# Kernel optimization log

Hardware: AMD Instinct MI355X
Metric: run time of the kernel (lower is better)

## Reference

```python
import jax, jax.numpy as jnp
import numpy as np

DIM = 1024
E = 8
N = 4096
HID = 4 * DIM
THRESHOLD = 0.3


def setup_inputs() -> dict:
    key = jax.random.key(0)
    ks = jax.random.split(key, 8)
    s = 0.02
    return {
        "x": jax.random.normal(ks[0], (N, DIM), dtype=jnp.float32),
        "expert_inputs": jax.random.normal(ks[1], (E, N, DIM), dtype=jnp.float32),
        "wg": jax.random.normal(ks[2], (DIM, E), dtype=jnp.float32) * s,
        "bg": jnp.zeros((E,), dtype=jnp.float32),
        "w1": jax.random.normal(ks[3], (E, DIM, HID), dtype=jnp.float32) * s,
        "b1": jnp.zeros((E, HID), dtype=jnp.float32),
        "w2": jax.random.normal(ks[4], (E, HID, DIM), dtype=jnp.float32) * s,
        "b2": jnp.zeros((E, DIM), dtype=jnp.float32),
    }


def reference(x, expert_inputs, wg, bg, w1, b1, w2, b2):
    # Gate: softmax over experts. [N, E]
    gate_scores = jax.nn.softmax(x @ wg + bg, axis=-1)

    # Experts: FeedForward(dim, dim, mult=4) = Linear -> GELU -> Linear, batched over E.
    h = jax.nn.gelu(jnp.einsum('end,edh->enh', expert_inputs, w1) + b1[:, None, :],
                    approximate=False)  # [E, N, HID]
    expert_outputs = jnp.einsum('enh,ehd->end', h, w2) + b2[:, None, :]  # [E, N, D]
    expert_outputs = jnp.transpose(expert_outputs, (1, 0, 2))  # [N, E, D]

    # Threshold mask + renormalized weighted combine.
    mask = gate_scores >= THRESHOLD
    masked_scores = gate_scores * mask.astype(gate_scores.dtype)
    normed = masked_scores / (masked_scores.sum(axis=1, keepdims=True) + 1e-6)
    fused = jnp.einsum('ne,ned->nd', normed, expert_outputs)  # [N, D]

    # Fallback: rows with no expert above threshold take the top-1 expert output.
    top1 = jnp.argmax(gate_scores, axis=1)  # [N]
    fallback = jnp.take_along_axis(expert_outputs, top1[:, None, None], axis=1)[:, 0, :]
    fb_mask = (mask.sum(axis=1) == 0)[:, None]
    fused = jnp.where(fb_mask, fallback, fused)
    return fused, gate_scores
```

## Files before the change

kernel.cpp:

```cpp
#include <hip/hip_runtime.h>
#include <hip/hip_bf16.h>
#include <cstdint>

#define N_TOK 4096
#define DIM_  1024
#define HID_  4096
#define NEXP  8
#define HHALF 2048
#define CAP   (3 * N_TOK)

typedef __attribute__((ext_vector_type(8))) short short8;
typedef __attribute__((ext_vector_type(4))) float f32x4;

__device__ __forceinline__ unsigned short f32_to_bf16(float f) {
    union { float f; uint32_t u; } v;
    v.f = f;
    uint32_t r = (v.u + 0x7fffu + ((v.u >> 16) & 1u)) >> 16;
    return (unsigned short)r;
}

__device__ __forceinline__ float gelu_exact(float x) {
    return 0.5f * x * (1.0f + erff(x * 0.70710678118654752440f));
}

__device__ __forceinline__ void gl_lds16(const unsigned short* g, unsigned short* l) {
    __builtin_amdgcn_global_load_lds(
        (const __attribute__((address_space(1))) void*)g,
        (__attribute__((address_space(3))) void*)l, 16, 0, 0);
}

__global__ __launch_bounds__(256)
void zero_init_kernel(float* __restrict__ fused, int* __restrict__ cnt)
{
    const int b = blockIdx.x;
    if (b < N_TOK) {
        float4* p = (float4*)(fused + (size_t)b * DIM_);
        p[threadIdx.x] = make_float4(0.f, 0.f, 0.f, 0.f);
    } else if (threadIdx.x < NEXP) {
        cnt[threadIdx.x] = 0;
    }
}

__global__ __launch_bounds__(256)
void gate_kernel(const float* __restrict__ x, const float* __restrict__ wg,
                 const float* __restrict__ bg, float* __restrict__ gates,
                 float* __restrict__ wts, int* __restrict__ cnt)
{
    const int wave = threadIdx.x >> 6;
    const int lane = threadIdx.x & 63;
    const int n = blockIdx.x * 4 + wave;
    float acc[NEXP];
#pragma unroll
    for (int e = 0; e < NEXP; e++) acc[e] = 0.0f;
    const float4* xr = (const float4*)(x + (size_t)n * DIM_);
#pragma unroll
    for (int j = 0; j < 4; j++) {
        const int k4 = lane + j * 64;
        const float4 v = xr[k4];
        const float* wr = wg + (size_t)k4 * 4 * NEXP;
#pragma unroll
        for (int e = 0; e < NEXP; e++)
            acc[e] += v.x * wr[e] + v.y * wr[NEXP + e] +
                      v.z * wr[2 * NEXP + e] + v.w * wr[3 * NEXP + e];
    }
#pragma unroll
    for (int e = 0; e < NEXP; e++) {
#pragma unroll
        for (int off = 32; off > 0; off >>= 1)
            acc[e] += __shfl_xor(acc[e], off, 64);
    }
    if (lane == 0) {
        float z[NEXP];
#pragma unroll
        for (int e = 0; e < NEXP; e++) z[e] = acc[e] + bg[e];
        float m = z[0];
#pragma unroll
        for (int e = 1; e < NEXP; e++) m = fmaxf(m, z[e]);
        float p[NEXP], s = 0.0f;
#pragma unroll
        for (int e = 0; e < NEXP; e++) { p[e] = __expf(z[e] - m); s += p[e]; }
        const float invs = 1.0f / s;
        float g[NEXP];
        int top = 0;
#pragma unroll
        for (int e = 0; e < NEXP; e++) {
            g[e] = p[e] * invs;
            gates[(size_t)n * NEXP + e] = g[e];
            if (g[e] > g[top]) top = e;
        }
        float w[NEXP], sm = 0.0f;
        int c = 0;
#pragma unroll
        for (int e = 0; e < NEXP; e++) {
            const bool mk = (g[e] >= 0.3f);
            const float ms = mk ? g[e] : 0.0f;
            sm += ms; c += mk ? 1 : 0;
            w[e] = ms;
        }
        if (c == 0) {
#pragma unroll
            for (int e = 0; e < NEXP; e++) w[e] = 0.0f;
            w[top] = 1.0f;
        } else {
            const float inv = 1.0f / (sm + 1e-6f);
#pragma unroll
            for (int e = 0; e < NEXP; e++) w[e] *= inv;
        }
#pragma unroll
        for (int e = 0; e < NEXP; e++) {
            wts[(size_t)n * NEXP + e] = w[e];
            if (w[e] > 0.0f) atomicAdd(&cnt[e], 1);
        }
    }
}

__global__ void offsets_kernel(const int* __restrict__ cnt, int* __restrict__ off,
                               int* __restrict__ cnt2)
{
    if (threadIdx.x == 0) {
        int a = 0;
        for (int e = 0; e < NEXP; e++) { off[e] = a; a += cnt[e]; cnt2[e] = 0; }
    }
}

__global__ __launch_bounds__(256)
void build_list_kernel(const float* __restrict__ wts, const int* __restrict__ off,
                       int* __restrict__ cnt2, int* __restrict__ gidx,
                       float* __restrict__ wpk)
{
    const int n = blockIdx.x * 256 + threadIdx.x;
    if (n >= N_TOK) return;
#pragma unroll
    for (int e = 0; e < NEXP; e++) {
        const float w = wts[(size_t)n * NEXP + e];
        if (w > 0.0f) {
            const int slot = atomicAdd(&cnt2[e], 1);
            const int g = off[e] + slot;
            gidx[g] = n;
            wpk[g] = w;
        }
    }
}

__global__ __launch_bounds__(256)
void gather_cvt_kernel(const float* __restrict__ ei, const int* __restrict__ cnt,
                       const int* __restrict__ off, const int* __restrict__ gidx,
                       unsigned short* __restrict__ xg)
{
    const int e = blockIdx.y;
    const int ne = cnt[e];
    const int i0 = blockIdx.x * 8;
    if (i0 >= ne) return;
    const int grp = threadIdx.x >> 5;
    const int l32 = threadIdx.x & 31;
    const int i = i0 + grp;
    if (i >= ne) return;
    const int o = off[e];
    const float* src = ei + ((size_t)e * N_TOK + gidx[o + i]) * DIM_;
    unsigned short* dst = xg + (size_t)(o + i) * DIM_;
#pragma unroll
    for (int j = 0; j < 8; j++) {
        const int c = (l32 + j * 32) * 4;
        const float4 v = *(const float4*)(src + c);
        ushort4 u;
        u.x = f32_to_bf16(v.x); u.y = f32_to_bf16(v.y);
        u.z = f32_to_bf16(v.z); u.w = f32_to_bf16(v.w);
        *(ushort4*)(dst + c) = u;
    }
}

__global__ __launch_bounds__(256)
void transpose_cvt3(const float* __restrict__ w1, const float* __restrict__ w2,
                    unsigned short* __restrict__ w1t, unsigned short* __restrict__ w2t)
{
    __shared__ __align__(16) unsigned short t[64 * 64];
    const int z = blockIdx.y;
    const float* src;
    unsigned short* dst;
    int C, R, cb, rb;
    if (z < NEXP) {
        src = w1 + (size_t)z * DIM_ * HID_;
        dst = w1t + (size_t)z * DIM_ * HID_;
        C = HID_; R = DIM_;
        cb = blockIdx.x & 63; rb = blockIdx.x >> 6;
    } else {
        src = w2 + (size_t)(z - NEXP) * HID_ * DIM_;
        dst = w2t + (size_t)(z - NEXP) * HID_ * DIM_;
        C = DIM_; R = HID_;
        cb = blockIdx.x & 15; rb = blockIdx.x >> 4;
    }
    const int c0 = cb * 64, r0 = rb * 64;
    const int tid = threadIdx.x;

    const int rB = (tid >> 4) * 4;
    const int cB = (tid & 15) * 4;
    float vv[4][4];
#pragma unroll
    for (int p = 0; p < 4; p++) {
        const float4 v = *(const float4*)(src + (size_t)(r0 + rB + p) * C + c0 + cB);
        vv[p][0] = v.x; vv[p][1] = v.y; vv[p][2] = v.z; vv[p][3] = v.w;
    }
#pragma unroll
    for (int k = 0; k < 4; k++) {
        const int c = cB + k;
        const int s = (c >> 3) & 7;
        const int addr = c * 64 + (((rB >> 3) ^ s) << 3) + (rB & 7);
        ushort4 q;
        q.x = f32_to_bf16(vv[0][k]);
        q.y = f32_to_bf16(vv[1][k]);
        q.z = f32_to_bf16(vv[2][k]);
        q.w = f32_to_bf16(vv[3][k]);
        *(ushort4*)(t + addr) = q;
    }
    __syncthreads();
#pragma unroll
    for (int it = 0; it < 2; it++) {
        const int c = (tid >> 3) + it * 32;
        const int g = tid & 7;
        const int s = (c >> 3) & 7;
        const short8 v8 = *(const short8*)(t + c * 64 + ((g ^ s) << 3));
        *(short8*)(dst + (size_t)(c0 + c) * R + r0 + g * 8) = v8;
    }
}

__global__ __launch_bounds__(256)
void gemm1_k(const unsigned short* __restrict__ xg, const unsigned short* __restrict__ w1t,
             const float* __restrict__ b1, unsigned short* __restrict__ hg,
             const int* __restrict__ cnt, const int* __restrict__ off, int h0)
{
    const int e = blockIdx.z;
    const int ne = cnt[e];
    const int rowBase = blockIdx.y * 128;
    if (rowBase >= ne) return;
    const int o = off[e];
    const int colBase = blockIdx.x * 128;

    __shared__ __align__(16) unsigned short sA[128 * 32];
    __shared__ __align__(16) unsigned short sB[128 * 32];
    const int tid  = threadIdx.x;
    const int lane = tid & 63;
    const int wave = tid >> 6;
    const int wr = wave >> 1, wc = wave & 1;

    f32x4 acc[4][4];
#pragma unroll
    for (int i = 0; i < 4; i++)
#pragma unroll
        for (int j = 0; j < 4; j++)
#pragma unroll
            for (int r = 0; r < 4; r++) acc[i][j][r] = 0.0f;

    const int sr = tid >> 2;
    const int sc = (tid & 3) << 3;
    const int rowA0 = min(rowBase + sr, ne - 1);
    const int rowA1 = min(rowBase + 64 + sr, ne - 1);
    const unsigned short* ga0 = xg + (size_t)(o + rowA0) * DIM_ + sc;
    const unsigned short* ga1 = xg + (size_t)(o + rowA1) * DIM_ + sc;
    const unsigned short* gb0 = w1t + ((size_t)e * HID_ + h0 + colBase + sr) * DIM_ + sc;
    const unsigned short* gb1 = gb0 + (size_t)64 * DIM_;
    unsigned short* la0 = sA + tid * 8;
    unsigned short* la1 = sA + 2048 + tid * 8;
    unsigned short* lb0 = sB + tid * 8;
    unsigned short* lb1 = sB + 2048 + tid * 8;

    const int aoff = (wr * 64 + (lane & 15)) * 32 + ((lane >> 4) << 3);
    const int boff = (wc * 64 + (lane & 15)) * 32 + ((lane >> 4) << 3);

    for (int k0 = 0; k0 < DIM_; k0 += 32) {
        gl_lds16(ga0 + k0, la0);
        gl_lds16(ga1 + k0, la1);
        gl_lds16(gb0 + k0, lb0);
        gl_lds16(gb1 + k0, lb1);
        __syncthreads();
        short8 av[4], bv[4];
#pragma unroll
        for (int i = 0; i < 4; i++) av[i] = *(const short8*)(sA + aoff + i * 16 * 32);
#pragma unroll
        for (int j = 0; j < 4; j++) bv[j] = *(const short8*)(sB + boff + j * 16 * 32);
#pragma unroll
        for (int i = 0; i < 4; i++)
#pragma unroll
            for (int j = 0; j < 4; j++)
                acc[i][j] = __builtin_amdgcn_mfma_f32_16x16x32_bf16(av[i], bv[j], acc[i][j], 0, 0, 0);
        __syncthreads();
    }

    const int crow = rowBase + wr * 64 + ((lane >> 4) << 2);
    const int ccol = colBase + wc * 64 + (lane & 15);
#pragma unroll
    for (int i = 0; i < 4; i++) {
#pragma unroll
        for (int j = 0; j < 4; j++) {
            const int col = ccol + j * 16;
            const float b = b1[(size_t)e * HID_ + h0 + col];
#pragma unroll
            for (int r = 0; r < 4; r++) {
                const int row = crow + i * 16 + r;
                if (row < ne) {
                    const float v = acc[i][j][r] + b;
                    hg[(size_t)(o + row) * HHALF + col] = f32_to_bf16(gelu_exact(v));
                }
            }
        }
    }
}

__global__ __launch_bounds__(256)
void gemm2_k(const unsigned short* __restrict__ hg, const unsigned short* __restrict__ w2t,
             const float* __restrict__ b2, float* __restrict__ fused,
             const int* __restrict__ cnt, const int* __restrict__ off,
             const int* __restrict__ gidx, const float* __restrict__ wpk, int h0)
{
    const int e = blockIdx.z;
    const int ne = cnt[e];
    const int rowBase = blockIdx.y * 128;
    if (rowBase >= ne) return;
    const int o = off[e];
    const int colBase = (blockIdx.x & 7) * 128;
    const int kc = blockIdx.x >> 3;
    const int kbeg = kc * (HHALF / 2);

    __shared__ __align__(16) unsigned short sA[128 * 32];
    __shared__ __align__(16) unsigned short sB[128 * 32];
    const int tid  = threadIdx.x;
    const int lane = tid & 63;
    const int wave = tid >> 6;
    const int wr = wave >> 1, wc = wave & 1;

    f32x4 acc[4][4];
#pragma unroll
    for (int i = 0; i < 4; i++)
#pragma unroll
        for (int j = 0; j < 4; j++)
#pragma unroll
            for (int r = 0; r < 4; r++) acc[i][j][r] = 0.0f;

    const int sr = tid >> 2;
    const int sc = (tid & 3) << 3;
    const int rowA0 = min(rowBase + sr, ne - 1);
    const int rowA1 = min(rowBase + 64 + sr, ne - 1);
    const unsigned short* ga0 = hg + (size_t)(o + rowA0) * HHALF + kbeg + sc;
    const unsigned short* ga1 = hg + (size_t)(o + rowA1) * HHALF + kbeg + sc;
    const unsigned short* gb0 = w2t + ((size_t)e * DIM_ + colBase + sr) * HID_ + h0 + kbeg + sc;
    const unsigned short* gb1 = gb0 + (size_t)64 * HID_;
    unsigned short* la0 = sA + tid * 8;
    unsigned short* la1 = sA + 2048 + tid * 8;
    unsigned short* lb0 = sB + tid * 8;
    unsigned short* lb1 = sB + 2048 + tid * 8;

    const int aoff = (wr * 64 + (lane & 15)) * 32 + ((lane >> 4) << 3);
    const int boff = (wc * 64 + (lane & 15)) * 32 + ((lane >> 4) << 3);

    for (int k0 = 0; k0 < HHALF / 2; k0 += 32) {
        gl_lds16(ga0 + k0, la0);
        gl_lds16(ga1 + k0, la1);
        gl_lds16(gb0 + k0, lb0);
        gl_lds16(gb1 + k0, lb1);
        __syncthreads();
        short8 av[4], bv[4];
#pragma unroll
        for (int i = 0; i < 4; i++) av[i] = *(const short8*)(sA + aoff + i * 16 * 32);
#pragma unroll
        for (int j = 0; j < 4; j++) bv[j] = *(const short8*)(sB + boff + j * 16 * 32);
#pragma unroll
        for (int i = 0; i < 4; i++)
#pragma unroll
            for (int j = 0; j < 4; j++)
                acc[i][j] = __builtin_amdgcn_mfma_f32_16x16x32_bf16(av[i], bv[j], acc[i][j], 0, 0, 0);
        __syncthreads();
    }

    const int crow = rowBase + wr * 64 + ((lane >> 4) << 2);
    const int ccol = colBase + wc * 64 + (lane & 15);
    const int addBias = (h0 == 0 && kc == 0);
#pragma unroll
    for (int i = 0; i < 4; i++) {
#pragma unroll
        for (int j = 0; j < 4; j++) {
            const int col = ccol + j * 16;
            const float b = addBias ? b2[(size_t)e * DIM_ + col] : 0.0f;
#pragma unroll
            for (int r = 0; r < 4; r++) {
                const int row = crow + i * 16 + r;
                if (row < ne) {
                    const float w = wpk[o + row];
                    const int orow = gidx[o + row];
                    atomicAdd(&fused[(size_t)orow * DIM_ + col], w * (acc[i][j][r] + b));
                }
            }
        }
    }
}

extern "C" void kernel_launch(void* const* d_in, const int* in_sizes, int n_in,
                              void* d_out, int out_size, void* d_ws, size_t ws_size,
                              hipStream_t stream)
{
    const float* x  = (const float*)d_in[0];
    const float* ei = (const float*)d_in[1];
    const float* wg = (const float*)d_in[2];
    const float* bg = (const float*)d_in[3];
    const float* w1 = (const float*)d_in[4];
    const float* b1 = (const float*)d_in[5];
    const float* w2 = (const float*)d_in[6];
    const float* b2 = (const float*)d_in[7];

    float* fused = (float*)d_out;
    float* gates = fused + (size_t)N_TOK * DIM_;

    unsigned short* xg  = (unsigned short*)d_ws;
    unsigned short* hg  = xg  + (size_t)CAP * DIM_;
    unsigned short* w1t = hg  + (size_t)CAP * HHALF;
    unsigned short* w2t = w1t + (size_t)NEXP * HID_ * DIM_;
    float* wts = (float*)(w2t + (size_t)NEXP * DIM_ * HID_);
    float* wpk = wts + (size_t)N_TOK * NEXP;
    int* gidx  = (int*)(wpk + CAP);
    int* cnt   = gidx + CAP;
    int* off   = cnt + NEXP;
    int* cnt2  = off + NEXP;

    zero_init_kernel<<<N_TOK + 1, 256, 0, stream>>>(fused, cnt);
    gate_kernel<<<N_TOK / 4, 256, 0, stream>>>(x, wg, bg, gates, wts, cnt);
    offsets_kernel<<<1, 64, 0, stream>>>(cnt, off, cnt2);
    build_list_kernel<<<N_TOK / 256, 256, 0, stream>>>(wts, off, cnt2, gidx, wpk);

    gather_cvt_kernel<<<dim3(N_TOK / 8, NEXP), 256, 0, stream>>>(ei, cnt, off, gidx, xg);
    transpose_cvt3<<<dim3(1024, 16), 256, 0, stream>>>(w1, w2, w1t, w2t);

    for (int h0 = 0; h0 < HID_; h0 += HHALF) {
        gemm1_k<<<dim3(HHALF / 128, N_TOK / 128, NEXP), 256, 0, stream>>>(
            xg, w1t, b1, hg, cnt, off, h0);
        gemm2_k<<<dim3(16, N_TOK / 128, NEXP), 256, 0, stream>>>(
            hg, w2t, b2, fused, cnt, off, gidx, wpk, h0);
    }
}
```

Before: 677.6 us.

## Double-buffer LDS in expert GEMMs and batch four tiles per transpose block

Both expert GEMM kernels now use two LDS buffers, so the async global-to-LDS loads for the next K slice are issued before the MFMAs on the current slice, with an explicit vmcnt wait and barrier. The aim is to overlap global memory latency with matrix compute instead of stalling on every K step. Separately, the weight transpose/convert kernel has each block handle four 64x64 tiles, with all loads issued up front and a quarter as many blocks launched, to raise memory-level parallelism per block. The cost is doubled LDS use per GEMM block, which may lower occupancy, and hand-written waitcnt logic that relies on how the compiler orders the loads.

```diff
diff --git a/kernel.cpp b/kernel.cpp
--- a/kernel.cpp
+++ b/kernel.cpp
@@ -177,49 +177,58 @@
     const int z = blockIdx.y;
     const float* src;
     unsigned short* dst;
-    int C, R, cb, rb;
+    int C, R, cmask, cshift;
     if (z < NEXP) {
         src = w1 + (size_t)z * DIM_ * HID_;
         dst = w1t + (size_t)z * DIM_ * HID_;
-        C = HID_; R = DIM_;
-        cb = blockIdx.x & 63; rb = blockIdx.x >> 6;
+        C = HID_; R = DIM_; cmask = 63; cshift = 6;
     } else {
         src = w2 + (size_t)(z - NEXP) * HID_ * DIM_;
         dst = w2t + (size_t)(z - NEXP) * HID_ * DIM_;
-        C = DIM_; R = HID_;
-        cb = blockIdx.x & 15; rb = blockIdx.x >> 4;
-    }
-    const int c0 = cb * 64, r0 = rb * 64;
+        C = DIM_; R = HID_; cmask = 15; cshift = 4;
+    }
     const int tid = threadIdx.x;
-
     const int rB = (tid >> 4) * 4;
     const int cB = (tid & 15) * 4;
-    float vv[4][4];
-#pragma unroll
-    for (int p = 0; p < 4; p++) {
-        const float4 v = *(const float4*)(src + (size_t)(r0 + rB + p) * C + c0 + cB);
-        vv[p][0] = v.x; vv[p][1] = v.y; vv[p][2] = v.z; vv[p][3] = v.w;
-    }
-#pragma unroll
-    for (int k = 0; k < 4; k++) {
-        const int c = cB + k;
-        const int s = (c >> 3) & 7;
-        const int addr = c * 64 + (((rB >> 3) ^ s) << 3) + (rB & 7);
-        ushort4 q;
-        q.x = f32_to_bf16(vv[0][k]);
-        q.y = f32_to_bf16(vv[1][k]);
-        q.z = f32_to_bf16(vv[2][k]);
-        q.w = f32_to_bf16(vv[3][k]);
-        *(ushort4*)(t + addr) = q;
-    }
-    __syncthreads();
-#pragma unroll
-    for (int it = 0; it < 2; it++) {
-        const int c = (tid >> 3) + it * 32;
-        const int g = tid & 7;
-        const int s = (c >> 3) & 7;
-        const short8 v8 = *(const short8*)(t + c * 64 + ((g ^ s) << 3));
-        *(short8*)(dst + (size_t)(c0 + c) * R + r0 + g * 8) = v8;
+
+    int c0[4], r0[4];
+#pragma unroll
+    for (int tt = 0; tt < 4; tt++) {
+        const int id = blockIdx.x * 4 + tt;
+        c0[tt] = (id & cmask) * 64;
+        r0[tt] = (id >> cshift) * 64;
+    }
+    f32x4 rr[4][4];
+#pragma unroll
+    for (int tt = 0; tt < 4; tt++)
+#pragma unroll
+        for (int p = 0; p < 4; p++)
+            rr[tt][p] = *(const f32x4*)(src + (size_t)(r0[tt] + rB + p) * C + c0[tt] + cB);
+
+#pragma unroll
+    for (int tt = 0; tt < 4; tt++) {
+        if (tt) __syncthreads();
+#pragma unroll
+        for (int k = 0; k < 4; k++) {
+            const int c = cB + k;
+            const int s = (c >> 3) & 7;
+            const int addr = c * 64 + (((rB >> 3) ^ s) << 3) + (rB & 7);
+            ushort4 q;
+            q.x = f32_to_bf16(rr[tt][0][k]);
+            q.y = f32_to_bf16(rr[tt][1][k]);
+            q.z = f32_to_bf16(rr[tt][2][k]);
+            q.w = f32_to_bf16(rr[tt][3][k]);
+            *(ushort4*)(t + addr) = q;
+        }
+        __syncthreads();
+#pragma unroll
+        for (int it2 = 0; it2 < 2; it2++) {
+            const int c = (tid >> 3) + it2 * 32;
+            const int g = tid & 7;
+            const int s = (c >> 3) & 7;
+            const short8 v8 = *(const short8*)(t + c * 64 + ((g ^ s) << 3));
+            *(short8*)(dst + (size_t)(c0[tt] + c) * R + r0[tt] + g * 8) = v8;
+        }
     }
 }
 
@@ -235,8 +244,8 @@
     const int o = off[e];
     const int colBase = blockIdx.x * 128;
 
-    __shared__ __align__(16) unsigned short sA[128 * 32];
-    __shared__ __align__(16) unsigned short sB[128 * 32];
+    __shared__ __align__(16) unsigned short sA[2][128 * 32];
+    __shared__ __align__(16) unsigned short sB[2][128 * 32];
     const int tid  = threadIdx.x;
     const int lane = tid & 63;
     const int wave = tid >> 6;
@@ -258,31 +267,36 @@
     const unsigned short* ga1 = xg + (size_t)(o + rowA1) * DIM_ + sc;
     const unsigned short* gb0 = w1t + ((size_t)e * HID_ + h0 + colBase + sr) * DIM_ + sc;
     const unsigned short* gb1 = gb0 + (size_t)64 * DIM_;
-    unsigned short* la0 = sA + tid * 8;
-    unsigned short* la1 = sA + 2048 + tid * 8;
-    unsigned short* lb0 = sB + tid * 8;
-    unsigned short* lb1 = sB + 2048 + tid * 8;
 
     const int aoff = (wr * 64 + (lane & 15)) * 32 + ((lane >> 4) << 3);
     const int boff = (wc * 64 + (lane & 15)) * 32 + ((lane >> 4) << 3);
 
-    for (int k0 = 0; k0 < DIM_; k0 += 32) {
-        gl_lds16(ga0 + k0, la0);
-        gl_lds16(ga1 + k0, la1);
-        gl_lds16(gb0 + k0, lb0);
-        gl_lds16(gb1 + k0, lb1);
-        __syncthreads();
+    gl_lds16(ga0, &sA[0][tid * 8]);
+    gl_lds16(ga1, &sA[0][2048 + tid * 8]);
+    gl_lds16(gb0, &sB[0][tid * 8]);
+    gl_lds16(gb1, &sB[0][2048 + tid * 8]);
+
+    const int NK = DIM_ / 32;
+    for (int it = 0; it < NK; ++it) {
+        const int cur = it & 1;
+        const int nxt = cur ^ 1;
+        const int kn = (it + 1 < NK) ? (it + 1) * 32 : it * 32;
+        gl_lds16(ga0 + kn, &sA[nxt][tid * 8]);
+        gl_lds16(ga1 + kn, &sA[nxt][2048 + tid * 8]);
+        gl_lds16(gb0 + kn, &sB[nxt][tid * 8]);
+        gl_lds16(gb1 + kn, &sB[nxt][2048 + tid * 8]);
+        asm volatile("s_waitcnt vmcnt(4)\n\ts_barrier" ::: "memory");
         short8 av[4], bv[4];
 #pragma unroll
-        for (int i = 0; i < 4; i++) av[i] = *(const short8*)(sA + aoff + i * 16 * 32);
-#pragma unroll
-        for (int j = 0; j < 4; j++) bv[j] = *(const short8*)(sB + boff + j * 16 * 32);
+        for (int i = 0; i < 4; i++) av[i] = *(const short8*)(&sA[cur][aoff + i * 16 * 32]);
+#pragma unroll
+        for (int j = 0; j < 4; j++) bv[j] = *(const short8*)(&sB[cur][boff + j * 16 * 32]);
 #pragma unroll
         for (int i = 0; i < 4; i++)
 #pragma unroll
             for (int j = 0; j < 4; j++)
                 acc[i][j] = __builtin_amdgcn_mfma_f32_16x16x32_bf16(av[i], bv[j], acc[i][j], 0, 0, 0);
-        __syncthreads();
+        asm volatile("s_barrier" ::: "memory");
     }
 
     const int crow = rowBase + wr * 64 + ((lane >> 4) << 2);
@@ -320,8 +334,8 @@
     const int kc = blockIdx.x >> 3;
     const int kbeg = kc * (HHALF / 2);
 
-    __shared__ __align__(16) unsigned short sA[128 * 32];
-    __shared__ __align__(16) unsigned short sB[128 * 32];
+    __shared__ __align__(16) unsigned short sA[2][128 * 32];
+    __shared__ __align__(16) unsigned short sB[2][128 * 32];
     const int tid  = threadIdx.x;
     const int lane = tid & 63;
     const int wave = tid >> 6;
@@ -343,31 +357,36 @@
     const unsigned short* ga1 = hg + (size_t)(o + rowA1) * HHALF + kbeg + sc;
     const unsigned short* gb0 = w2t + ((size_t)e * DIM_ + colBase + sr) * HID_ + h0 + kbeg + sc;
     const unsigned short* gb1 = gb0 + (size_t)64 * HID_;
-    unsigned short* la0 = sA + tid * 8;
-    unsigned short* la1 = sA + 2048 + tid * 8;
-    unsigned short* lb0 = sB + tid * 8;
-    unsigned short* lb1 = sB + 2048 + tid * 8;
 
     const int aoff = (wr * 64 + (lane & 15)) * 32 + ((lane >> 4) << 3);
     const int boff = (wc * 64 + (lane & 15)) * 32 + ((lane >> 4) << 3);
 
-    for (int k0 = 0; k0 < HHALF / 2; k0 += 32) {
-        gl_lds16(ga0 + k0, la0);
-        gl_lds16(ga1 + k0, la1);
-        gl_lds16(gb0 + k0, lb0);
-        gl_lds16(gb1 + k0, lb1);
-        __syncthreads();
+    gl_lds16(ga0, &sA[0][tid * 8]);
+    gl_lds16(ga1, &sA[0][2048 + tid * 8]);
+    gl_lds16(gb0, &sB[0][tid * 8]);
+    gl_lds16(gb1, &sB[0][2048 + tid * 8]);
+
+    const int NK = (HHALF / 2) / 32;
+    for (int it = 0; it < NK; ++it) {
+        const int cur = it & 1;
+        const int nxt = cur ^ 1;
+        const int kn = (it + 1 < NK) ? (it + 1) * 32 : it * 32;
+        gl_lds16(ga0 + kn, &sA[nxt][tid * 8]);
+        gl_lds16(ga1 + kn, &sA[nxt][2048 + tid * 8]);
+        gl_lds16(gb0 + kn, &sB[nxt][tid * 8]);
+        gl_lds16(gb1 + kn, &sB[nxt][2048 + tid * 8]);
+        asm volatile("s_waitcnt vmcnt(4)\n\ts_barrier" ::: "memory");
         short8 av[4], bv[4];
 #pragma unroll
-        for (int i = 0; i < 4; i++) av[i] = *(const short8*)(sA + aoff + i * 16 * 32);
-#pragma unroll
-        for (int j = 0; j < 4; j++) bv[j] = *(const short8*)(sB + boff + j * 16 * 32);
+        for (int i = 0; i < 4; i++) av[i] = *(const short8*)(&sA[cur][aoff + i * 16 * 32]);
+#pragma unroll
+        for (int j = 0; j < 4; j++) bv[j] = *(const short8*)(&sB[cur][boff + j * 16 * 32]);
 #pragma unroll
         for (int i = 0; i < 4; i++)
 #pragma unroll
             for (int j = 0; j < 4; j++)
                 acc[i][j] = __builtin_amdgcn_mfma_f32_16x16x32_bf16(av[i], bv[j], acc[i][j], 0, 0, 0);
-        __syncthreads();
+        asm volatile("s_barrier" ::: "memory");
     }
 
     const int crow = rowBase + wr * 64 + ((lane >> 4) << 2);
@@ -425,7 +444,7 @@
     build_list_kernel<<<N_TOK / 256, 256, 0, stream>>>(wts, off, cnt2, gidx, wpk);
 
     gather_cvt_kernel<<<dim3(N_TOK / 8, NEXP), 256, 0, stream>>>(ei, cnt, off, gidx, xg);
-    transpose_cvt3<<<dim3(1024, 16), 256, 0, stream>>>(w1, w2, w1t, w2t);
+    transpose_cvt3<<<dim3(256, 16), 256, 0, stream>>>(w1, w2, w1t, w2t);
 
     for (int h0 = 0; h0 < HID_; h0 += HHALF) {
         gemm1_k<<<dim3(HHALF / 128, N_TOK / 128, NEXP), 256, 0, stream>>>(
```

New measurement: 701.7 us. 1.04x slower.
